# Kernel tuning notes

Hardware: AMD Instinct MI355X
Metric: run time of the kernel (lower is better)

The kernel has to match this reference:

```python
import jax, jax.numpy as jnp
import numpy as np

N = 50000      # nodes
E = 800000     # edges (avg degree 16)
D_IN, D_H, D_OUT = 128, 96, 32


def _lin(x, W, b):
    return x @ W.T + b


def _transformer_conv(x, src, dst, Wq, bq, Wk, bk, Wv, bv, Ws, bs, n):
    # PyG TransformerConv, heads=1: q_i . k_j / sqrt(d), segment softmax over
    # incoming edges of each target node, weighted sum of values, plus skip.
    q = _lin(x, Wq, bq)            # [N, d]
    k = _lin(x, Wk, bk)            # [N, d]
    v = _lin(x, Wv, bv)            # [N, d]
    d = q.shape[-1]
    score = jnp.sum(q[dst] * k[src], axis=-1) / jnp.sqrt(jnp.float32(d))  # [E]
    m = jax.ops.segment_max(score, dst, num_segments=n)                   # [N]
    m = jnp.where(jnp.isneginf(m), 0.0, m)   # isolated nodes
    e = jnp.exp(score - m[dst])                                           # [E]
    denom = jax.ops.segment_sum(e, dst, num_segments=n)                   # [N]
    alpha = e / jnp.maximum(denom[dst], 1e-16)                            # [E]
    agg = jax.ops.segment_sum(alpha[:, None] * v[src], dst, num_segments=n)
    return agg + _lin(x, Ws, bs)   # root weight (skip connection)


def setup_inputs() -> dict:
    key = jax.random.key(0)
    ks = jax.random.split(key, 32)
    x = jax.random.normal(ks[0], (N, D_IN), dtype=jnp.float32)
    edge_index = jax.random.randint(ks[1], (2, E), 0, N, dtype=jnp.int64)
    dims = [(D_IN, D_H), (D_H, D_H), (D_H, D_OUT)]
    inp = {"x": x, "edge_index": edge_index}
    ki = 2
    for li, (fi, fo) in enumerate(dims, start=1):
        s = 1.0 / np.sqrt(fi)
        for nm in ("Wq", "Wk", "Wv", "Ws"):
            inp[f"{nm}{li}"] = jax.random.normal(ks[ki], (fo, fi), dtype=jnp.float32) * s
            ki += 1
        for nm in ("bq", "bk", "bv", "bs"):
            inp[f"{nm}{li}"] = jnp.zeros((fo,), dtype=jnp.float32)
    return inp


def reference(x, edge_index,
              Wq1, Wk1, Wv1, Ws1, bq1, bk1, bv1, bs1,
              Wq2, Wk2, Wv2, Ws2, bq2, bk2, bv2, bs2,
              Wq3, Wk3, Wv3, Ws3, bq3, bk3, bv3, bs3):
    src, dst = edge_index[0], edge_index[1]
    h = jax.nn.relu(_transformer_conv(x, src, dst, Wq1, bq1, Wk1, bk1, Wv1, bv1, Ws1, bs1, N))
    h = jax.nn.relu(_transformer_conv(h, src, dst, Wq2, bq2, Wk2, bk2, Wv2, bv2, Ws2, bs2, N))
    h = _transformer_conv(h, src, dst, Wq3, bq3, Wk3, bk3, Wv3, bv3, Ws3, bs3, N)
    return jax.nn.log_softmax(h, axis=1)
```

## Files before the change

### kernel.cpp

```cpp
#include <hip/hip_runtime.h>
#include <math.h>

typedef __attribute__((ext_vector_type(8))) __bf16 bf16x8;
typedef __attribute__((ext_vector_type(8))) short short8;
typedef __attribute__((ext_vector_type(4))) float f32x4;
typedef unsigned int uint;
typedef unsigned short ushort;
typedef unsigned char uchar;


__device__ inline bf16x8 ld_bf8(const ushort* p){
  short8 s = *reinterpret_cast<const short8*>(p);
  return __builtin_bit_cast(bf16x8, s);
}

__device__ inline ushort f2bf(float f){
  return __builtin_bit_cast(ushort, (__bf16)f);
}
__device__ inline uint pack2bf(float a, float b){
  return (uint)f2bf(a) | ((uint)f2bf(b) << 16);
}
__device__ inline float bf_lo(uint u){ return __builtin_bit_cast(float, u << 16); }
__device__ inline float bf_hi(uint u){ return __builtin_bit_cast(float, u & 0xFFFF0000u); }

template<int S>
__device__ inline float unp8(uint w){
  return __builtin_amdgcn_cvt_f32_fp8((int)w, S);
}
__device__ inline uint pk8(float a, float b, float c, float d){
  int r = 0;
  r = __builtin_amdgcn_cvt_pk_fp8_f32(a, b, r, false);
  r = __builtin_amdgcn_cvt_pk_fp8_f32(c, d, r, true);
  return (uint)r;
}


__global__ void k_zero(int* __restrict__ p, int n){
  if ((int)threadIdx.x < n) p[threadIdx.x] = 0;
}

__global__ __launch_bounds__(256) void k_bucketA(const int* __restrict__ dst,
                                                 int* __restrict__ gbh, int E){
  __shared__ int cnt[256];
  cnt[threadIdx.x] = 0;
  __syncthreads();
  for (int e = blockIdx.x * blockDim.x + threadIdx.x; e < E; e += gridDim.x * blockDim.x)
    atomicAdd(&cnt[dst[e] >> 8], 1);
  __syncthreads();
  int c = cnt[threadIdx.x];
  if (c > 0) atomicAdd(&gbh[threadIdx.x], c);
}

__global__ __launch_bounds__(256) void k_bscan(const int* __restrict__ gbh,
                                               int* __restrict__ gbase,
                                               int* __restrict__ gcur, int NB, int E){
  __shared__ int wsum[4];
  int t = threadIdx.x;
  int c = (t < NB) ? gbh[t] : 0;
  int lane = t & 63, wv = t >> 6;
  int incl = c;
  #pragma unroll
  for (int o = 1; o < 64; o <<= 1){
    int x = __shfl_up(incl, o);
    if (lane >= o) incl += x;
  }
  if (lane == 63) wsum[wv] = incl;
  __syncthreads();
  int woff = 0;
  for (int w = 0; w < wv; ++w) woff += wsum[w];
  int excl = woff + incl - c;
  if (t < NB){ gbase[t] = excl; gcur[t] = excl; }
  if (t == 0) gbase[NB] = E;
}

#define CS_CHUNK 4096
__global__ __launch_bounds__(256) void k_bucketB(const int* __restrict__ src,
                                                 const int* __restrict__ dst,
                                                 int* __restrict__ gcur,
                                                 uint* __restrict__ epack, int E){
  __shared__ int cnt[256];
  __shared__ int wcur[256];
  const int b0 = blockIdx.x * CS_CHUNK;
  const int b1 = (b0 + CS_CHUNK < E) ? b0 + CS_CHUNK : E;
  cnt[threadIdx.x] = 0;
  __syncthreads();
  for (int e = b0 + threadIdx.x; e < b1; e += 256)
    atomicAdd(&cnt[dst[e] >> 8], 1);
  __syncthreads();
  int c = cnt[threadIdx.x];
  int base = (c > 0) ? atomicAdd(&gcur[threadIdx.x], c) : 0;
  wcur[threadIdx.x] = base;
  __syncthreads();
  for (int e = b0 + threadIdx.x; e < b1; e += 256){
    int d = dst[e];
    int s = src[e];
    int pos = atomicAdd(&wcur[d >> 8], 1);
    epack[pos] = ((uint)d << 16) | (uint)(s & 0xFFFF);
  }
}

__global__ __launch_bounds__(256) void k_bucketC(const uint* __restrict__ epack,
                                                 const int* __restrict__ gbase,
                                                 int* __restrict__ offs,
                                                 ushort* __restrict__ srclist,
                                                 int N, int E){
  __shared__ int cnt[256];
  __shared__ int wcur[256];
  __shared__ int wsum[4];
  const int b = blockIdx.x;
  const int lo = gbase[b], hi = gbase[b + 1];
  cnt[threadIdx.x] = 0;
  __syncthreads();
  for (int i = lo + threadIdx.x; i < hi; i += 256)
    atomicAdd(&cnt[(epack[i] >> 16) & 255], 1);
  __syncthreads();
  int c = cnt[threadIdx.x];
  int lane = threadIdx.x & 63, wv = threadIdx.x >> 6;
  int incl = c;
  #pragma unroll
  for (int o = 1; o < 64; o <<= 1){
    int x = __shfl_up(incl, o);
    if (lane >= o) incl += x;
  }
  if (lane == 63) wsum[wv] = incl;
  __syncthreads();
  int woff = 0;
  for (int w = 0; w < wv; ++w) woff += wsum[w];
  int excl = lo + woff + incl - c;
  int d = (b << 8) + threadIdx.x;
  if (d < N) offs[d] = excl;
  wcur[threadIdx.x] = excl;
  __syncthreads();
  for (int i = lo + threadIdx.x; i < hi; i += 256){
    uint ep = epack[i];
    int pos = atomicAdd(&wcur[(ep >> 16) & 255], 1);
    srclist[pos] = (ushort)(ep & 0xFFFF);
  }
  if (b == 0 && threadIdx.x == 0) offs[N] = E;
}


struct WSet { const float* src[12]; ushort* dst[12]; int n[12]; };

__global__ __launch_bounds__(256) void k_castw(WSet ws){
  int m = blockIdx.y;
  int n = ws.n[m];
  const float* s = ws.src[m];
  ushort* d = ws.dst[m];
  for (int i = blockIdx.x * blockDim.x + threadIdx.x; i < n; i += gridDim.x * blockDim.x)
    d[i] = f2bf(s[i]);
}


template<int KT, int NT, bool F32IN>
__global__ __launch_bounds__(256) void k_projmfma(
    const ushort* __restrict__ hin, const float* __restrict__ hinf, int N,
    const ushort* __restrict__ Wq, const ushort* __restrict__ Wk,
    const ushort* __restrict__ Wv, const ushort* __restrict__ Wsk,
    const float* __restrict__ bq, const float* __restrict__ bk,
    const float* __restrict__ bv, const float* __restrict__ bs,
    ushort* __restrict__ qo, uchar* __restrict__ kv8,
    ushort* __restrict__ so, int kvstB)
{
  constexpr int K  = KT * 32;
  constexpr int PS = K + 8;
  constexpr int FO = NT * 16;
  __shared__ ushort wlds[FO * PS];

  const int mat = blockIdx.y;
  const ushort* W = (mat == 0) ? Wq : (mat == 1) ? Wk : (mat == 2) ? Wv : Wsk;
  const float*  b = (mat == 0) ? bq : (mat == 1) ? bk : (mat == 2) ? bv : bs;

  for (int idx = threadIdx.x; idx < FO * (K / 8); idx += 256){
    int row = idx / (K / 8);
    int c8  = idx - row * (K / 8);
    *reinterpret_cast<short8*>(&wlds[row * PS + c8 * 8]) =
        *reinterpret_cast<const short8*>(W + (size_t)row * K + c8 * 8);
  }
  __syncthreads();

  const int wv   = threadIdx.x >> 6;
  const int lane = threadIdx.x & 63;
  const int r16  = lane & 15;
  const int kg   = lane >> 4;

  float4 bias[NT];
  #pragma unroll
  for (int nt = 0; nt < NT; ++nt)
    bias[nt] = *reinterpret_cast<const float4*>(b + nt * 16 + kg * 4);

  const int MT = N >> 4;
  for (int mt = blockIdx.x * 4 + wv; mt < MT; mt += gridDim.x * 4){
    const int row0 = mt * 16;
    bf16x8 af[KT];
    #pragma unroll
    for (int kt = 0; kt < KT; ++kt){
      if constexpr (F32IN){
        const float* xr = hinf + (size_t)(row0 + r16) * K + kt * 32 + kg * 8;
        float4 a = reinterpret_cast<const float4*>(xr)[0];
        float4 c = reinterpret_cast<const float4*>(xr)[1];
        uint4 u;
        u.x = pack2bf(a.x, a.y); u.y = pack2bf(a.z, a.w);
        u.z = pack2bf(c.x, c.y); u.w = pack2bf(c.z, c.w);
        af[kt] = __builtin_bit_cast(bf16x8, u);
      } else {
        af[kt] = ld_bf8(hin + (size_t)(row0 + r16) * K + kt * 32 + kg * 8);
      }
    }

    f32x4 acc[NT];
    #pragma unroll
    for (int nt = 0; nt < NT; ++nt){
      acc[nt][0] = bias[nt].x; acc[nt][1] = bias[nt].y;
      acc[nt][2] = bias[nt].z; acc[nt][3] = bias[nt].w;
    }
    #pragma unroll
    for (int nt = 0; nt < NT; ++nt)
      #pragma unroll
      for (int kt = 0; kt < KT; ++kt){
        bf16x8 bfr = ld_bf8(&wlds[(nt * 16 + r16) * PS + kt * 32 + kg * 8]);
        acc[nt] = __builtin_amdgcn_mfma_f32_16x16x32_bf16(bfr, af[kt], acc[nt], 0, 0, 0);
      }

    const int row = row0 + r16;
    if (mat == 0 || mat == 3){
      ushort* out = (mat == 0) ? qo : so;
      #pragma unroll
      for (int nt = 0; nt < NT; ++nt){
        uint* p = reinterpret_cast<uint*>(out + (size_t)row * FO + nt * 16 + kg * 4);
        p[0] = pack2bf(acc[nt][0], acc[nt][1]);
        p[1] = pack2bf(acc[nt][2], acc[nt][3]);
      }
    } else {
      const int voff = (mat == 2) ? FO : 0;
      #pragma unroll
      for (int nt = 0; nt < NT; ++nt){
        uint u = pk8(acc[nt][0], acc[nt][1], acc[nt][2], acc[nt][3]);
        *reinterpret_cast<uint*>(kv8 + (size_t)row * kvstB + voff + nt * 16 + kg * 4) = u;
      }
    }
  }
}


template<int FO, int MODE>
__global__ __launch_bounds__(256) void k_attn3(
    const ushort* __restrict__ qb, const uchar* __restrict__ kv,
    const ushort* __restrict__ skipb, const int* __restrict__ offs,
    const ushort* __restrict__ srclist, void* __restrict__ outp,
    int N, float scale)
{
  constexpr int G   = 8;
  constexpr int FPL = FO / G;
  constexpr int KW  = FPL / 4;
  constexpr int KVB = 2 * FO;
  const int lane = threadIdx.x & 63;
  const int sub  = lane & 7;
  const int node = (blockIdx.x * (blockDim.x >> 6) + (threadIdx.x >> 6)) * 8 + (lane >> 3);
  const bool nv  = node < N;
  const int nodec = nv ? node : 0;

  const uint2* qrow = reinterpret_cast<const uint2*>(qb + (size_t)nodec * FO + sub * FPL);
  float qf[FPL];
  #pragma unroll
  for (int w = 0; w < KW; ++w){
    uint2 t = qrow[w];
    qf[4 * w]     = bf_lo(t.x); qf[4 * w + 1] = bf_hi(t.x);
    qf[4 * w + 2] = bf_lo(t.y); qf[4 * w + 3] = bf_hi(t.y);
  }

  float m = -INFINITY, l = 0.f;
  float acc[FPL];
  #pragma unroll
  for (int f = 0; f < FPL; ++f) acc[f] = 0.f;

  const int e0 = nv ? offs[node] : 0;
  const int e1 = nv ? offs[node + 1] : 0;

  uint kA[4][KW], vA[4][KW], kB[4][KW], vB[4][KW];

  auto DOLOAD = [&](int eb, uint (*Kr)[KW], uint (*Vr)[KW]){
    #pragma unroll
    for (int i = 0; i < 4; ++i){
      int ee = eb + i;
      int ec = (ee < e1) ? ee : (e1 - 1);
      int j = srclist[ec];
      const uchar* row = kv + (size_t)j * KVB;
      const uint* rk = reinterpret_cast<const uint*>(row + sub * FPL);
      const uint* rv = reinterpret_cast<const uint*>(row + FO + sub * FPL);
      #pragma unroll
      for (int w = 0; w < KW; ++w){
        Kr[i][w] = rk[w];
        Vr[i][w] = rv[w];
      }
    }
  };

  auto COMPUTE = [&](uint (*Kr)[KW], uint (*Vr)[KW], int ebase){
    float s[4];
    #pragma unroll
    for (int i = 0; i < 4; ++i){
      float t = 0.f;
      #pragma unroll
      for (int w = 0; w < KW; ++w){
        uint kwd = Kr[i][w];
        t = fmaf(qf[4 * w],     unp8<0>(kwd), t);
        t = fmaf(qf[4 * w + 1], unp8<1>(kwd), t);
        t = fmaf(qf[4 * w + 2], unp8<2>(kwd), t);
        t = fmaf(qf[4 * w + 3], unp8<3>(kwd), t);
      }
      s[i] = t;
    }
    #pragma unroll
    for (int o = 1; o < G; o <<= 1){
      s[0] += __shfl_xor(s[0], o);
      s[1] += __shfl_xor(s[1], o);
      s[2] += __shfl_xor(s[2], o);
      s[3] += __shfl_xor(s[3], o);
    }
    s[0] = s[0] * scale;
    s[1] = (ebase + 1 < e1) ? s[1] * scale : -1e30f;
    s[2] = (ebase + 2 < e1) ? s[2] * scale : -1e30f;
    s[3] = (ebase + 3 < e1) ? s[3] * scale : -1e30f;

    float mnew = fmaxf(fmaxf(m, s[0]), fmaxf(fmaxf(s[1], s[2]), s[3]));
    float sfac = __expf(m - mnew);
    float p4[4];
    p4[0] = __expf(s[0] - mnew);
    p4[1] = __expf(s[1] - mnew);
    p4[2] = __expf(s[2] - mnew);
    p4[3] = __expf(s[3] - mnew);
    l = l * sfac + (p4[0] + p4[1]) + (p4[2] + p4[3]);
    #pragma unroll
    for (int f = 0; f < FPL; ++f) acc[f] *= sfac;
    #pragma unroll
    for (int i = 0; i < 4; ++i){
      #pragma unroll
      for (int w = 0; w < KW; ++w){
        uint vwd = Vr[i][w];
        acc[4 * w]     = fmaf(p4[i], unp8<0>(vwd), acc[4 * w]);
        acc[4 * w + 1] = fmaf(p4[i], unp8<1>(vwd), acc[4 * w + 1]);
        acc[4 * w + 2] = fmaf(p4[i], unp8<2>(vwd), acc[4 * w + 2]);
        acc[4 * w + 3] = fmaf(p4[i], unp8<3>(vwd), acc[4 * w + 3]);
      }
    }
    m = mnew;
  };

  if (e0 < e1){
    int e = e0;
    DOLOAD(e, kA, vA);
    for (;;){
      int en = e + 4;
      bool more = en < e1;
      if (more) DOLOAD(en, kB, vB);
      COMPUTE(kA, vA, e);
      e = en;
      if (!more) break;
      en = e + 4;
      more = en < e1;
      if (more) DOLOAD(en, kA, vA);
      COMPUTE(kB, vB, e);
      e = en;
      if (!more) break;
    }
  }

  float inv = 1.f / fmaxf(l, 1e-16f);
  const uint2* srow = reinterpret_cast<const uint2*>(skipb + (size_t)nodec * FO + sub * FPL);
  float val[FPL];
  #pragma unroll
  for (int w = 0; w < KW; ++w){
    uint2 t = srow[w];
    val[4 * w]     = bf_lo(t.x) + acc[4 * w] * inv;
    val[4 * w + 1] = bf_hi(t.x) + acc[4 * w + 1] * inv;
    val[4 * w + 2] = bf_lo(t.y) + acc[4 * w + 2] * inv;
    val[4 * w + 3] = bf_hi(t.y) + acc[4 * w + 3] * inv;
  }

  if (MODE == 0){
    if (nv){
      uint2* orow = reinterpret_cast<uint2*>((ushort*)outp + (size_t)node * FO + sub * FPL);
      #pragma unroll
      for (int w = 0; w < KW; ++w){
        uint2 o;
        o.x = pack2bf(fmaxf(val[4 * w], 0.f),     fmaxf(val[4 * w + 1], 0.f));
        o.y = pack2bf(fmaxf(val[4 * w + 2], 0.f), fmaxf(val[4 * w + 3], 0.f));
        orow[w] = o;
      }
    }
  } else {
    float mx = -INFINITY;
    #pragma unroll
    for (int f = 0; f < FPL; ++f) mx = fmaxf(mx, val[f]);
    #pragma unroll
    for (int o = 1; o < G; o <<= 1) mx = fmaxf(mx, __shfl_xor(mx, o));
    float ssum = 0.f;
    #pragma unroll
    for (int f = 0; f < FPL; ++f) ssum += __expf(val[f] - mx);
    #pragma unroll
    for (int o = 1; o < G; o <<= 1) ssum += __shfl_xor(ssum, o);
    float lg = __logf(ssum);
    if (nv){
      float* orow = (float*)outp + (size_t)node * FO + sub * FPL;
      #pragma unroll
      for (int f = 0; f < FPL; ++f) orow[f] = val[f] - mx - lg;
    }
  }
}


extern "C" void kernel_launch(void* const* d_in, const int* in_sizes, int n_in,
                              void* d_out, int out_size, void* d_ws, size_t ws_size,
                              hipStream_t stream)
{
  const float* x  = (const float*)d_in[0];
  const int*   ei = (const int*)d_in[1];
  const int N = in_sizes[0] / 128;
  const int E = in_sizes[1] / 2;

  const float* W1[4]; const float* b1[4];
  const float* W2[4]; const float* b2[4];
  const float* W3[4]; const float* b3[4];
  for (int i = 0; i < 4; ++i){
    W1[i] = (const float*)d_in[2 + i];   b1[i] = (const float*)d_in[6 + i];
    W2[i] = (const float*)d_in[10 + i];  b2[i] = (const float*)d_in[14 + i];
    W3[i] = (const float*)d_in[18 + i];  b3[i] = (const float*)d_in[22 + i];
  }

  size_t off = 0;
  auto alloc = [&](size_t bytes) -> void* {
    void* p = (char*)d_ws + off;
    off = (off + bytes + 255) & ~(size_t)255;
    return p;
  };
  const int NB = (N + 255) / 256;
  int* offs       = (int*)alloc(((size_t)N + 1) * 4);
  int* gbh        = (int*)alloc(256 * 4);
  int* gbase      = (int*)alloc(260 * 4);
  int* gcur       = (int*)alloc(256 * 4);
  uint* epack     = (uint*)alloc((size_t)E * 4);
  ushort* srclist = (ushort*)alloc((size_t)E * 2);
  ushort* qb  = (ushort*)alloc((size_t)N * 96 * 2);
  uchar*  kvb = (uchar*)alloc((size_t)N * 192);
  ushort* sb  = (ushort*)alloc((size_t)N * 96 * 2);
  ushort* hb  = (ushort*)alloc((size_t)N * 128 * 2);
  ushort* wb  = (ushort*)alloc((size_t)98304 * 2);

  ushort* Wb1[4]; ushort* Wb2[4]; ushort* Wb3[4];
  for (int i = 0; i < 4; ++i){
    Wb1[i] = wb + (size_t)i * 12288;
    Wb2[i] = wb + 49152 + (size_t)i * 9216;
    Wb3[i] = wb + 49152 + 36864 + (size_t)i * 3072;
  }

  WSet wset;
  for (int i = 0; i < 4; ++i){
    wset.src[i]     = W1[i]; wset.dst[i]     = Wb1[i]; wset.n[i]     = 12288;
    wset.src[4 + i] = W2[i]; wset.dst[4 + i] = Wb2[i]; wset.n[4 + i] = 9216;
    wset.src[8 + i] = W3[i]; wset.dst[8 + i] = Wb3[i]; wset.n[8 + i] = 3072;
  }
  k_castw<<<dim3(48, 12), dim3(256), 0, stream>>>(wset);

  const int* esrc = ei;
  const int* edst = ei + E;
  k_zero<<<dim3(1), dim3(256), 0, stream>>>(gbh, 256);
  k_bucketA<<<dim3(392), dim3(256), 0, stream>>>(edst, gbh, E);
  k_bscan<<<dim3(1), dim3(256), 0, stream>>>(gbh, gbase, gcur, NB, E);
  const int nCB = (E + CS_CHUNK - 1) / CS_CHUNK;
  k_bucketB<<<dim3(nCB), dim3(256), 0, stream>>>(esrc, edst, gcur, epack, E);
  k_bucketC<<<dim3(NB), dim3(256), 0, stream>>>(epack, gbase, offs, srclist, N, E);

  float* outf = (float*)d_out;
  const float sc96 = 1.0f / sqrtf(96.f);
  const float sc32 = 1.0f / sqrtf(32.f);

  const int gridA = (N + 31) / 32;

  k_projmfma<4, 6, true><<<dim3(384, 4), dim3(256), 0, stream>>>(nullptr, x, N,
      Wb1[0], Wb1[1], Wb1[2], Wb1[3], b1[0], b1[1], b1[2], b1[3],
      qb, kvb, sb, 192);
  k_attn3<96, 0><<<dim3(gridA), dim3(256), 0, stream>>>(qb, kvb, sb, offs, srclist, hb, N, sc96);

  k_projmfma<3, 6, false><<<dim3(384, 4), dim3(256), 0, stream>>>(hb, nullptr, N,
      Wb2[0], Wb2[1], Wb2[2], Wb2[3], b2[0], b2[1], b2[2], b2[3],
      qb, kvb, sb, 192);
  k_attn3<96, 0><<<dim3(gridA), dim3(256), 0, stream>>>(qb, kvb, sb, offs, srclist, hb, N, sc96);

  k_projmfma<3, 2, false><<<dim3(384, 4), dim3(256), 0, stream>>>(hb, nullptr, N,
      Wb3[0], Wb3[1], Wb3[2], Wb3[3], b3[0], b3[1], b3[2], b3[3],
      qb, kvb, sb, 64);
  k_attn3<32, 1><<<dim3(gridA), dim3(256), 0, stream>>>(qb, kvb, sb, offs, srclist, outf, N, sc32);
}
```

Before: 186.0 us.

## Restructure projection GEMM to stage input rows in LDS, one wave per weight

The projection kernel previously loaded one weight matrix into LDS per block and looped over row tiles, reading the input activations once per matrix. Now each block stages a 32-row input tile into LDS once. Each of the four waves computes one of Q/K/V/skip for that tile, reading weight fragments straight from global memory or cache. This cuts input reads fourfold and removes the grid-stride loop, at the cost of redundant weight reads per block. Separately, zeroing the bucket histogram is folded into the weight-cast launch, which drops one kernel launch.

```diff
diff --git a/kernel.cpp b/kernel.cpp
--- a/kernel.cpp
+++ b/kernel.cpp
@@ -34,10 +34,6 @@
   return (uint)r;
 }
 
-
-__global__ void k_zero(int* __restrict__ p, int n){
-  if ((int)threadIdx.x < n) p[threadIdx.x] = 0;
-}
 
 __global__ __launch_bounds__(256) void k_bucketA(const int* __restrict__ dst,
                                                  int* __restrict__ gbh, int E){
@@ -142,8 +138,12 @@
 
 struct WSet { const float* src[12]; ushort* dst[12]; int n[12]; };
 
-__global__ __launch_bounds__(256) void k_castw(WSet ws){
+__global__ __launch_bounds__(256) void k_castw(WSet ws, int* __restrict__ gbh){
   int m = blockIdx.y;
+  if (m == 12){
+    if (blockIdx.x == 0) gbh[threadIdx.x] = 0;
+    return;
+  }
   int n = ws.n[m];
   const float* s = ws.src[m];
   ushort* d = ws.dst[m];
@@ -153,7 +153,7 @@
 
 
 template<int KT, int NT, bool F32IN>
-__global__ __launch_bounds__(256) void k_projmfma(
+__global__ __launch_bounds__(256) void k_proj(
     const ushort* __restrict__ hin, const float* __restrict__ hinf, int N,
     const ushort* __restrict__ Wq, const ushort* __restrict__ Wk,
     const ushort* __restrict__ Wv, const ushort* __restrict__ Wsk,
@@ -163,80 +163,89 @@
     ushort* __restrict__ so, int kvstB)
 {
   constexpr int K  = KT * 32;
-  constexpr int PS = K + 8;
+  constexpr int PS = K + 16;
   constexpr int FO = NT * 16;
-  __shared__ ushort wlds[FO * PS];
-
-  const int mat = blockIdx.y;
-  const ushort* W = (mat == 0) ? Wq : (mat == 1) ? Wk : (mat == 2) ? Wv : Wsk;
-  const float*  b = (mat == 0) ? bq : (mat == 1) ? bk : (mat == 2) ? bv : bs;
-
-  for (int idx = threadIdx.x; idx < FO * (K / 8); idx += 256){
-    int row = idx / (K / 8);
-    int c8  = idx - row * (K / 8);
-    *reinterpret_cast<short8*>(&wlds[row * PS + c8 * 8]) =
-        *reinterpret_cast<const short8*>(W + (size_t)row * K + c8 * 8);
-  }
-  __syncthreads();
-
-  const int wv   = threadIdx.x >> 6;
+  __shared__ ushort alds[32 * PS];
+
+  const int row0 = blockIdx.x * 32;
+
+  for (int idx = threadIdx.x; idx < 32 * (K / 8); idx += 256){
+    int r  = idx / (K / 8);
+    int c8 = idx - r * (K / 8);
+    int rr = row0 + r; if (rr >= N) rr = N - 1;
+    if constexpr (F32IN){
+      const float* xr = hinf + (size_t)rr * K + c8 * 8;
+      float4 a = reinterpret_cast<const float4*>(xr)[0];
+      float4 c = reinterpret_cast<const float4*>(xr)[1];
+      uint4 u;
+      u.x = pack2bf(a.x, a.y); u.y = pack2bf(a.z, a.w);
+      u.z = pack2bf(c.x, c.y); u.w = pack2bf(c.z, c.w);
+      *reinterpret_cast<uint4*>(&alds[r * PS + c8 * 8]) = u;
+    } else {
+      *reinterpret_cast<short8*>(&alds[r * PS + c8 * 8]) =
+          *reinterpret_cast<const short8*>(hin + (size_t)rr * K + c8 * 8);
+    }
+  }
+  __syncthreads();
+
+  const int mat  = threadIdx.x >> 6;
   const int lane = threadIdx.x & 63;
   const int r16  = lane & 15;
   const int kg   = lane >> 4;
 
-  float4 bias[NT];
-  #pragma unroll
-  for (int nt = 0; nt < NT; ++nt)
-    bias[nt] = *reinterpret_cast<const float4*>(b + nt * 16 + kg * 4);
-
-  const int MT = N >> 4;
-  for (int mt = blockIdx.x * 4 + wv; mt < MT; mt += gridDim.x * 4){
-    const int row0 = mt * 16;
-    bf16x8 af[KT];
+  const ushort* W = (mat == 0) ? Wq : (mat == 1) ? Wk : (mat == 2) ? Wv : Wsk;
+  const float*  b = (mat == 0) ? bq : (mat == 1) ? bk : (mat == 2) ? bv : bs;
+
+  bf16x8 af[2][KT];
+  #pragma unroll
+  for (int m = 0; m < 2; ++m)
+    #pragma unroll
+    for (int kt = 0; kt < KT; ++kt)
+      af[m][kt] = ld_bf8(&alds[(m * 16 + r16) * PS + kt * 32 + kg * 8]);
+
+  f32x4 acc[2][NT];
+  #pragma unroll
+  for (int nt = 0; nt < NT; ++nt){
+    float4 bb = *reinterpret_cast<const float4*>(b + nt * 16 + kg * 4);
+    #pragma unroll
+    for (int m = 0; m < 2; ++m){
+      acc[m][nt][0] = bb.x; acc[m][nt][1] = bb.y;
+      acc[m][nt][2] = bb.z; acc[m][nt][3] = bb.w;
+    }
+  }
+
+  #pragma unroll
+  for (int nt = 0; nt < NT; ++nt){
+    bf16x8 wf[KT];
+    #pragma unroll
+    for (int kt = 0; kt < KT; ++kt)
+      wf[kt] = ld_bf8(W + (size_t)(nt * 16 + r16) * K + kt * 32 + kg * 8);
     #pragma unroll
     for (int kt = 0; kt < KT; ++kt){
-      if constexpr (F32IN){
-        const float* xr = hinf + (size_t)(row0 + r16) * K + kt * 32 + kg * 8;
-        float4 a = reinterpret_cast<const float4*>(xr)[0];
-        float4 c = reinterpret_cast<const float4*>(xr)[1];
-        uint4 u;
-        u.x = pack2bf(a.x, a.y); u.y = pack2bf(a.z, a.w);
-        u.z = pack2bf(c.x, c.y); u.w = pack2bf(c.z, c.w);
-        af[kt] = __builtin_bit_cast(bf16x8, u);
+      acc[0][nt] = __builtin_amdgcn_mfma_f32_16x16x32_bf16(wf[kt], af[0][kt], acc[0][nt], 0, 0, 0);
+      acc[1][nt] = __builtin_amdgcn_mfma_f32_16x16x32_bf16(wf[kt], af[1][kt], acc[1][nt], 0, 0, 0);
+    }
+  }
+
+  #pragma unroll
+  for (int m = 0; m < 2; ++m){
+    const int row = row0 + m * 16 + r16;
+    if (row < N){
+      if (mat == 0 || mat == 3){
+        ushort* out = (mat == 0) ? qo : so;
+        #pragma unroll
+        for (int nt = 0; nt < NT; ++nt){
+          uint* p = reinterpret_cast<uint*>(out + (size_t)row * FO + nt * 16 + kg * 4);
+          p[0] = pack2bf(acc[m][nt][0], acc[m][nt][1]);
+          p[1] = pack2bf(acc[m][nt][2], acc[m][nt][3]);
+        }
       } else {
-        af[kt] = ld_bf8(hin + (size_t)(row0 + r16) * K + kt * 32 + kg * 8);
-      }
-    }
-
-    f32x4 acc[NT];
-    #pragma unroll
-    for (int nt = 0; nt < NT; ++nt){
-      acc[nt][0] = bias[nt].x; acc[nt][1] = bias[nt].y;
-      acc[nt][2] = bias[nt].z; acc[nt][3] = bias[nt].w;
-    }
-    #pragma unroll
-    for (int nt = 0; nt < NT; ++nt)
-      #pragma unroll
-      for (int kt = 0; kt < KT; ++kt){
-        bf16x8 bfr = ld_bf8(&wlds[(nt * 16 + r16) * PS + kt * 32 + kg * 8]);
-        acc[nt] = __builtin_amdgcn_mfma_f32_16x16x32_bf16(bfr, af[kt], acc[nt], 0, 0, 0);
-      }
-
-    const int row = row0 + r16;
-    if (mat == 0 || mat == 3){
-      ushort* out = (mat == 0) ? qo : so;
-      #pragma unroll
-      for (int nt = 0; nt < NT; ++nt){
-        uint* p = reinterpret_cast<uint*>(out + (size_t)row * FO + nt * 16 + kg * 4);
-        p[0] = pack2bf(acc[nt][0], acc[nt][1]);
-        p[1] = pack2bf(acc[nt][2], acc[nt][3]);
-      }
-    } else {
-      const int voff = (mat == 2) ? FO : 0;
-      #pragma unroll
-      for (int nt = 0; nt < NT; ++nt){
-        uint u = pk8(acc[nt][0], acc[nt][1], acc[nt][2], acc[nt][3]);
-        *reinterpret_cast<uint*>(kv8 + (size_t)row * kvstB + voff + nt * 16 + kg * 4) = u;
+        const int voff = (mat == 2) ? FO : 0;
+        #pragma unroll
+        for (int nt = 0; nt < NT; ++nt){
+          uint u = pk8(acc[m][nt][0], acc[m][nt][1], acc[m][nt][2], acc[m][nt][3]);
+          *reinterpret_cast<uint*>(kv8 + (size_t)row * kvstB + voff + nt * 16 + kg * 4) = u;
+        }
       }
     }
   }
@@ -460,11 +469,10 @@
     wset.src[4 + i] = W2[i]; wset.dst[4 + i] = Wb2[i]; wset.n[4 + i] = 9216;
     wset.src[8 + i] = W3[i]; wset.dst[8 + i] = Wb3[i]; wset.n[8 + i] = 3072;
   }
-  k_castw<<<dim3(48, 12), dim3(256), 0, stream>>>(wset);
+  k_castw<<<dim3(48, 13), dim3(256), 0, stream>>>(wset, gbh);
 
   const int* esrc = ei;
   const int* edst = ei + E;
-  k_zero<<<dim3(1), dim3(256), 0, stream>>>(gbh, 256);
   k_bucketA<<<dim3(392), dim3(256), 0, stream>>>(edst, gbh, E);
   k_bscan<<<dim3(1), dim3(256), 0, stream>>>(gbh, gbase, gcur, NB, E);
   const int nCB = (E + CS_CHUNK - 1) / CS_CHUNK;
@@ -475,19 +483,20 @@
   const float sc96 = 1.0f / sqrtf(96.f);
   const float sc32 = 1.0f / sqrtf(32.f);
 
+  const int gridP = (N + 31) / 32;
   const int gridA = (N + 31) / 32;
 
-  k_projmfma<4, 6, true><<<dim3(384, 4), dim3(256), 0, stream>>>(nullptr, x, N,
+  k_proj<4, 6, true><<<dim3(gridP), dim3(256), 0, stream>>>(nullptr, x, N,
       Wb1[0], Wb1[1], Wb1[2], Wb1[3], b1[0], b1[1], b1[2], b1[3],
       qb, kvb, sb, 192);
   k_attn3<96, 0><<<dim3(gridA), dim3(256), 0, stream>>>(qb, kvb, sb, offs, srclist, hb, N, sc96);
 
-  k_projmfma<3, 6, false><<<dim3(384, 4), dim3(256), 0, stream>>>(hb, nullptr, N,
+  k_proj<3, 6, false><<<dim3(gridP), dim3(256), 0, stream>>>(hb, nullptr, N,
       Wb2[0], Wb2[1], Wb2[2], Wb2[3], b2[0], b2[1], b2[2], b2[3],
       qb, kvb, sb, 192);
   k_attn3<96, 0><<<dim3(gridA), dim3(256), 0, stream>>>(qb, kvb, sb, offs, srclist, hb, N, sc96);
 
-  k_projmfma<3, 2, false><<<dim3(384, 4), dim3(256), 0, stream>>>(hb, nullptr, N,
+  k_proj<3, 2, false><<<dim3(gridP), dim3(256), 0, stream>>>(hb, nullptr, N,
       Wb3[0], Wb3[1], Wb3[2], Wb3[3], b3[0], b3[1], b3[2], b3[3],
       qb, kvb, sb, 64);
   k_attn3<32, 1><<<dim3(gridA), dim3(256), 0, stream>>>(qb, kvb, sb, offs, srclist, outf, N, sc32);
```

Result: slower. 193.4 us (+4.0%).
